# Kernel tuning notes

Hardware: AMD Instinct MI355X
Metric: run time of the kernel (lower is better)

Reference implementation:

```python
import jax, jax.numpy as jnp
import numpy as np

DIM = 768
N_HEADS = 12
HEAD_DIM = DIM // N_HEADS
HIDDEN = 4 * DIM
EPS = 1e-5


def _layernorm(x, g, b):
    m = jnp.mean(x, axis=-1, keepdims=True)
    v = jnp.mean(jnp.square(x - m), axis=-1, keepdims=True)
    return (x - m) * jax.lax.rsqrt(v + EPS) * g + b


def setup_inputs() -> dict:
    key = jax.random.key(0)
    ks = jax.random.split(key, 16)
    s = lambda fan_in: 1.0 / np.sqrt(fan_in)
    return {
        "x": jax.random.normal(ks[0], (2, 2048, DIM), dtype=jnp.float32),
        "ln1_g": jnp.ones((DIM,), jnp.float32),
        "ln1_b": jnp.zeros((DIM,), jnp.float32),
        "qkv_w": jax.random.uniform(ks[1], (DIM, 3 * DIM), jnp.float32, -s(DIM), s(DIM)),
        "qkv_b": jax.random.uniform(ks[2], (3 * DIM,), jnp.float32, -s(DIM), s(DIM)),
        "proj_w": jax.random.uniform(ks[3], (DIM, DIM), jnp.float32, -s(DIM), s(DIM)),
        "proj_b": jax.random.uniform(ks[4], (DIM,), jnp.float32, -s(DIM), s(DIM)),
        "ln2_g": jnp.ones((DIM,), jnp.float32),
        "ln2_b": jnp.zeros((DIM,), jnp.float32),
        "w1": jax.random.uniform(ks[5], (DIM, HIDDEN), jnp.float32, -s(DIM), s(DIM)),
        "b1": jax.random.uniform(ks[6], (HIDDEN,), jnp.float32, -s(DIM), s(DIM)),
        "w2": jax.random.uniform(ks[7], (HIDDEN, DIM), jnp.float32, -s(HIDDEN), s(HIDDEN)),
        "b2": jax.random.uniform(ks[8], (DIM,), jnp.float32, -s(HIDDEN), s(HIDDEN)),
    }


def reference(x, ln1_g, ln1_b, qkv_w, qkv_b, proj_w, proj_b, ln2_g, ln2_b, w1, b1, w2, b2):
    B, N, C = x.shape
    # ---- attention branch (pre-norm) ----
    h = _layernorm(x, ln1_g, ln1_b)
    qkv = (h @ qkv_w + qkv_b).reshape(B, N, 3, N_HEADS, HEAD_DIM)
    qkv = qkv.transpose(2, 0, 3, 1, 4)  # [3, B, H, N, Dh]
    q, k, v = qkv[0], qkv[1], qkv[2]
    scale = HEAD_DIM ** -0.5
    scores = jnp.einsum("bhnd,bhmd->bhnm", q, k) * scale  # [B,H,N,N]
    attn = jax.nn.softmax(scores, axis=-1)
    ctx = jnp.einsum("bhnm,bhmd->bhnd", attn, v)  # [B,H,N,Dh]
    ctx = ctx.transpose(0, 2, 1, 3).reshape(B, N, C)
    x = x + ctx @ proj_w + proj_b
    # ---- MLP branch (pre-norm) ----
    h = _layernorm(x, ln2_g, ln2_b)
    h = jax.nn.gelu(h @ w1 + b1, approximate=False)  # torch nn.GELU default = exact erf
    x = x + h @ w2 + b2
    return x
```

## Files before the change

### kernel.cpp

```cpp
#include <hip/hip_runtime.h>
#include <hip/hip_bf16.h>
#include <math.h>

#define DIM 768
#define NHEADS 12
#define HDIM 64
#define HIDDEN 3072
#define SEQ 2048
#define NTOK 4096
#define QKV3 2304

typedef __attribute__((ext_vector_type(8))) __bf16 bf16x8;
typedef __attribute__((ext_vector_type(4))) float f32x4;
typedef __attribute__((ext_vector_type(16))) float f32x16;

__device__ __forceinline__ ushort f32_bf16(float f) {
  union { float f; uint u; } c{f};
  uint u = c.u;
  u = (u + 0x7FFFu + ((u >> 16) & 1u)) >> 16;
  return (ushort)u;
}

__device__ __forceinline__ uint cvt_pk_bf16(float lo, float hi) {
  uint r;
  asm("v_cvt_pk_bf16_f32 %0, %1, %2" : "=v"(r) : "v"(lo), "v"(hi));
  return r;
}

__device__ __forceinline__ void glds16(const ushort* g, ushort* l) {
  __builtin_amdgcn_global_load_lds(
      (const __attribute__((address_space(1))) unsigned int*)(const void*)g,
      (__attribute__((address_space(3))) unsigned int*)(void*)l, 16, 0, 0);
}

union U8 { uint u[4]; bf16x8 v; };

__global__ __launch_bounds__(256) void transpose_to_bf16(
    const float* __restrict__ in, ushort* __restrict__ out, int K, int N) {
  __shared__ float tile[32][33];
  int kb = blockIdx.y * 32, nb = blockIdx.x * 32;
  int tx = threadIdx.x, ty = threadIdx.y;
#pragma unroll
  for (int i = 0; i < 32; i += 8)
    tile[ty + i][tx] = in[(size_t)(kb + ty + i) * N + nb + tx];
  __syncthreads();
#pragma unroll
  for (int i = 0; i < 32; i += 8)
    out[(size_t)(nb + ty + i) * K + kb + tx] = f32_bf16(tile[tx][ty + i]);
}

__global__ __launch_bounds__(256) void ln_bf16(
    const float* __restrict__ x, const float* __restrict__ g,
    const float* __restrict__ bta, ushort* __restrict__ out) {
  int row = blockIdx.x;
  const float* xr = x + (size_t)row * DIM;
  int t = threadIdx.x;
  float v0 = xr[t], v1 = xr[t + 256], v2 = xr[t + 512];
  float s = v0 + v1 + v2;
  float q = v0 * v0 + v1 * v1 + v2 * v2;
#pragma unroll
  for (int m = 1; m < 64; m <<= 1) {
    s += __shfl_xor(s, m);
    q += __shfl_xor(q, m);
  }
  __shared__ float ss[4], qq[4];
  int wid = t >> 6;
  if ((t & 63) == 0) { ss[wid] = s; qq[wid] = q; }
  __syncthreads();
  s = ss[0] + ss[1] + ss[2] + ss[3];
  q = qq[0] + qq[1] + qq[2] + qq[3];
  float mean = s * (1.0f / DIM);
  float var = q * (1.0f / DIM) - mean * mean;
  float rs = rsqrtf(var + 1e-5f);
  size_t o = (size_t)row * DIM;
  out[o + t]       = f32_bf16((v0 - mean) * rs * g[t]       + bta[t]);
  out[o + t + 256] = f32_bf16((v1 - mean) * rs * g[t + 256] + bta[t + 256]);
  out[o + t + 512] = f32_bf16((v2 - mean) * rs * g[t + 512] + bta[t + 512]);
}

template <int EPI>
__global__ __launch_bounds__(256, 2) void gemm_bf16(
    const ushort* __restrict__ A, const ushort* __restrict__ Bt,
    const float* __restrict__ bias, const float* __restrict__ resid,
    void* __restrict__ outv, int M, int N, int K) {
  __shared__ __align__(16) ushort As[128 * 64];
  __shared__ __align__(16) ushort Bs[128 * 64];
  int t = threadIdx.x;
  int lane = t & 63, w = t >> 6;
  int wr = w >> 1, wc = w & 1;
  int m0 = blockIdx.y * 128, n0 = blockIdx.x * 128;
  f32x4 acc[4][4] = {};
  int rl = lane & 15, g = lane >> 4, rl7 = rl & 7;

  int baseRow = w * 32 + (lane >> 3);
  int cs = (lane & 7) ^ ((lane >> 3) & 7);
  const ushort* Asrc = A + (size_t)(m0 + baseRow) * K + cs * 8;
  const ushort* Bsrc = Bt + (size_t)(n0 + baseRow) * K + cs * 8;
  ushort* Adst = &As[(w * 256 + lane) * 8];
  ushort* Bdst = &Bs[(w * 256 + lane) * 8];

  for (int k0 = 0; k0 < K; k0 += 64) {
    __syncthreads();
#pragma unroll
    for (int i = 0; i < 4; i++) {
      glds16(Asrc + (size_t)i * 8 * K + k0, Adst + i * 512);
      glds16(Bsrc + (size_t)i * 8 * K + k0, Bdst + i * 512);
    }
    __syncthreads();
    bf16x8 a[2][4], b[2][4];
#pragma unroll
    for (int kk = 0; kk < 2; kk++)
#pragma unroll
      for (int i = 0; i < 4; i++) {
        a[kk][i] = *(const bf16x8*)&As[(wr * 64 + i * 16 + rl) * 64 + ((kk * 4 + g) ^ rl7) * 8];
        b[kk][i] = *(const bf16x8*)&Bs[(wc * 64 + i * 16 + rl) * 64 + ((kk * 4 + g) ^ rl7) * 8];
      }
#pragma unroll
    for (int kk = 0; kk < 2; kk++)
#pragma unroll
      for (int i = 0; i < 4; i++)
#pragma unroll
        for (int j = 0; j < 4; j++)
          acc[i][j] = __builtin_amdgcn_mfma_f32_16x16x32_bf16(a[kk][i], b[kk][j], acc[i][j], 0, 0, 0);
  }
  int g4 = (lane >> 4) * 4;
#pragma unroll
  for (int i = 0; i < 4; i++) {
#pragma unroll
    for (int j = 0; j < 4; j++) {
      int col = n0 + wc * 64 + j * 16 + rl;
      float bval = bias[col];
#pragma unroll
      for (int r = 0; r < 4; r++) {
        int row = m0 + wr * 64 + i * 16 + g4 + r;
        float v = acc[i][j][r] + bval;
        if (EPI == 0) {
          ((ushort*)outv)[(size_t)row * N + col] = f32_bf16(v);
        } else if (EPI == 1) {
          v += resid[(size_t)row * N + col];
          ((float*)outv)[(size_t)row * N + col] = v;
        } else {
          v = 0.5f * v * (1.0f + erff(v * 0.70710678118654752f));
          ((ushort*)outv)[(size_t)row * N + col] = f32_bf16(v);
        }
      }
    }
  }
}

__global__ __launch_bounds__(256, 3) void attn_kernel(
    const ushort* __restrict__ qkv, ushort* __restrict__ ctx) {
  __shared__ __align__(16) ushort Ks[2][4096];
  __shared__ __align__(16) ushort Vt[2][4096];
  __shared__ float mml[2][2][64];
  int t = threadIdx.x, lane = t & 63, w = t >> 6;
  int qh = w & 1, kvpar = w >> 1;
  int kl = lane & 31, hi = lane >> 5;
  int qt = blockIdx.x, h = blockIdx.y, b = blockIdx.z;

  bf16x8 bq[4];
  {
    size_t qbase = (size_t)(b * SEQ + qt * 64 + qh * 32 + kl) * QKV3 + h * HDIM + hi * 8;
#pragma unroll
    for (int mi = 0; mi < 4; mi++) bq[mi] = *(const bf16x8*)(qkv + qbase + mi * 16);
  }
  f32x16 acc_o[2] = {};
  float m2 = -1e30f, lst = 0.0f;

  int pairLane = qh * 64 + lane;
  const ushort* kbase = qkv + (size_t)(b * SEQ) * QKV3 + DIM + h * HDIM;
  ushort* KsB = Ks[kvpar];
  ushort* VtB = Vt[kvpar];

  for (int it = 0; it < SEQ / 128; it++) {
    int kt = it * 2 + kvpar;
    __syncthreads();
#pragma unroll
    for (int i = 0; i < 4; i++) {
      int s = i * 128 + pairLane;
      int key = s >> 3, cc = s & 7;
      int c = cc ^ (key & 7);
      glds16(kbase + (size_t)(kt * 64 + key) * QKV3 + c * 8, &KsB[s * 8]);
    }
#pragma unroll
    for (int i = 0; i < 4; i++) {
      int s = i * 128 + pairLane;
      int key = s >> 3, c = s & 7;
      uint4 v4 = *(const uint4*)(kbase + DIM + (size_t)(kt * 64 + key) * QKV3 + c * 8);
      int co = ((key >> 3) ^ c) * 8 + (key & 7);
      uint vv[4] = {v4.x, v4.y, v4.z, v4.w};
#pragma unroll
      for (int u = 0; u < 4; u++) {
        VtB[(c * 8 + 2 * u) * 64 + co]     = (ushort)(vv[u] & 0xffffu);
        VtB[(c * 8 + 2 * u + 1) * 64 + co] = (ushort)(vv[u] >> 16);
      }
    }
    __syncthreads();

    f32x16 accs[2] = {};
#pragma unroll
    for (int ks = 0; ks < 2; ks++) {
      int key = ks * 32 + kl;
      int kswz = key & 7;
#pragma unroll
      for (int mi = 0; mi < 4; mi++) {
        bf16x8 ak = *(const bf16x8*)&KsB[key * 64 + ((2 * mi + hi) ^ kswz) * 8];
        accs[ks] = __builtin_amdgcn_mfma_f32_32x32x16_bf16(ak, bq[mi], accs[ks], 0, 0, 0);
      }
    }

    float mx = accs[0][0];
#pragma unroll
    for (int ks = 0; ks < 2; ks++)
#pragma unroll
      for (int r = 0; r < 16; r++) mx = fmaxf(mx, accs[ks][r]);
    mx = fmaxf(mx, __shfl_xor(mx, 32));
    float me = mx * 0.125f;
    if (!__all(me - m2 <= 8.0f)) {
      float newm = fmaxf(m2, me);
      float fac = __expf(m2 - newm);
      m2 = newm;
      lst *= fac;
#pragma unroll
      for (int r = 0; r < 16; r++) {
        int qrow = (r & 3) + 8 * (r >> 2) + 4 * hi;
        float fr = __shfl(fac, qrow | (lane & 32));
        acc_o[0][r] *= fr;
        acc_o[1][r] *= fr;
      }
    }
    float ps = 0.0f;
    uint PK[2][8];
#pragma unroll
    for (int ks = 0; ks < 2; ks++)
#pragma unroll
      for (int rp = 0; rp < 8; rp++) {
        float p0 = __expf(fmaf(accs[ks][2 * rp],     0.125f, -m2));
        float p1 = __expf(fmaf(accs[ks][2 * rp + 1], 0.125f, -m2));
        ps += p0 + p1;
        PK[ks][rp] = cvt_pk_bf16(p0, p1);
      }
    ps += __shfl_xor(ps, 32);
    lst += ps;

#pragma unroll
    for (int tt = 0; tt < 4; tt++) {
      const int ks = tt >> 1, tb = 4 * (tt & 1);
      uint e0 = hi ? PK[ks][tb]     : PK[ks][tb + 2];
      uint e1 = hi ? PK[ks][tb + 1] : PK[ks][tb + 3];
      uint x0 = __shfl_xor(e0, 32), x1 = __shfl_xor(e1, 32);
      uint l0 = hi ? PK[ks][tb + 2] : PK[ks][tb];
      uint l1 = hi ? PK[ks][tb + 3] : PK[ks][tb + 1];
      U8 a;
      a.u[0] = hi ? x0 : l0;
      a.u[1] = hi ? x1 : l1;
      a.u[2] = hi ? l0 : x0;
      a.u[3] = hi ? l1 : x1;
#pragma unroll
      for (int dn = 0; dn < 2; dn++) {
        int d = dn * 32 + kl;
        bf16x8 bv = *(const bf16x8*)&VtB[d * 64 + ((2 * tt + hi) ^ (d >> 3)) * 8];
        acc_o[dn] = __builtin_amdgcn_mfma_f32_32x32x16_bf16(a.v, bv, acc_o[dn], 0, 0, 0);
      }
    }
  }

  __syncthreads();
  float* obuf = (float*)(qh ? Ks[1] : Ks[0]);
  if (kvpar == 1) {
#pragma unroll
    for (int dn = 0; dn < 2; dn++)
#pragma unroll
      for (int r = 0; r < 16; r++)
        obuf[(dn * 16 + r) * 64 + lane] = acc_o[dn][r];
    mml[qh][0][lane] = m2;
    mml[qh][1][lane] = lst;
  }
  __syncthreads();
  if (kvpar == 0) {
    float mb = mml[qh][0][lane], lb = mml[qh][1][lane];
    float m = fmaxf(m2, mb);
    float fa = __expf(m2 - m), fb = __expf(mb - m);
    lst = lst * fa + lb * fb;
    float inv = 1.0f / lst;
#pragma unroll
    for (int r = 0; r < 16; r++) {
      int qrow = (r & 3) + 8 * (r >> 2) + 4 * hi;
      int src = qrow | (lane & 32);
      float far = __shfl(fa, src), fbr = __shfl(fb, src), ir = __shfl(inv, src);
      size_t row = (size_t)(b * SEQ + qt * 64 + qh * 32 + qrow);
#pragma unroll
      for (int dn = 0; dn < 2; dn++) {
        float v = (acc_o[dn][r] * far + obuf[(dn * 16 + r) * 64 + lane] * fbr) * ir;
        ctx[row * DIM + h * HDIM + dn * 32 + kl] = f32_bf16(v);
      }
    }
  }
}

extern "C" void kernel_launch(void* const* d_in, const int* in_sizes, int n_in,
                              void* d_out, int out_size, void* d_ws, size_t ws_size,
                              hipStream_t stream) {
  const float* x      = (const float*)d_in[0];
  const float* ln1_g  = (const float*)d_in[1];
  const float* ln1_b  = (const float*)d_in[2];
  const float* qkv_w  = (const float*)d_in[3];
  const float* qkv_b  = (const float*)d_in[4];
  const float* proj_w = (const float*)d_in[5];
  const float* proj_b = (const float*)d_in[6];
  const float* ln2_g  = (const float*)d_in[7];
  const float* ln2_b  = (const float*)d_in[8];
  const float* w1     = (const float*)d_in[9];
  const float* b1     = (const float*)d_in[10];
  const float* w2     = (const float*)d_in[11];
  const float* b2     = (const float*)d_in[12];
  float* out = (float*)d_out;

  char* ws = (char*)d_ws;
  size_t off = 0;
  auto alloc = [&](size_t bytes) -> void* {
    void* p = ws + off;
    off += (bytes + 255) & ~(size_t)255;
    return p;
  };
  ushort* wqkv_t  = (ushort*)alloc((size_t)QKV3 * DIM * 2);
  ushort* wproj_t = (ushort*)alloc((size_t)DIM * DIM * 2);
  ushort* w1_t    = (ushort*)alloc((size_t)HIDDEN * DIM * 2);
  ushort* w2_t    = (ushort*)alloc((size_t)DIM * HIDDEN * 2);
  ushort* hbuf    = (ushort*)alloc((size_t)NTOK * DIM * 2);
  ushort* ubuf    = (ushort*)alloc((size_t)NTOK * HIDDEN * 2);
  ushort* ctx     = (ushort*)alloc((size_t)NTOK * DIM * 2);
  float*  x1      = (float*)alloc((size_t)NTOK * DIM * 4);
  ushort* qkvbuf = ubuf;
  ushort* m1     = ubuf;

  transpose_to_bf16<<<dim3(QKV3 / 32, DIM / 32), dim3(32, 8), 0, stream>>>(qkv_w, wqkv_t, DIM, QKV3);
  transpose_to_bf16<<<dim3(DIM / 32, DIM / 32), dim3(32, 8), 0, stream>>>(proj_w, wproj_t, DIM, DIM);
  transpose_to_bf16<<<dim3(HIDDEN / 32, DIM / 32), dim3(32, 8), 0, stream>>>(w1, w1_t, DIM, HIDDEN);
  transpose_to_bf16<<<dim3(DIM / 32, HIDDEN / 32), dim3(32, 8), 0, stream>>>(w2, w2_t, HIDDEN, DIM);

  ln_bf16<<<NTOK, 256, 0, stream>>>(x, ln1_g, ln1_b, hbuf);
  gemm_bf16<0><<<dim3(QKV3 / 128, NTOK / 128), 256, 0, stream>>>(
      hbuf, wqkv_t, qkv_b, nullptr, qkvbuf, NTOK, QKV3, DIM);
  attn_kernel<<<dim3(SEQ / 64, NHEADS, 2), 256, 0, stream>>>(qkvbuf, ctx);
  gemm_bf16<1><<<dim3(DIM / 128, NTOK / 128), 256, 0, stream>>>(
      ctx, wproj_t, proj_b, x, x1, NTOK, DIM, DIM);
  ln_bf16<<<NTOK, 256, 0, stream>>>(x1, ln2_g, ln2_b, hbuf);
  gemm_bf16<2><<<dim3(HIDDEN / 128, NTOK / 128), 256, 0, stream>>>(
      hbuf, w1_t, b1, nullptr, m1, NTOK, HIDDEN, DIM);
  gemm_bf16<1><<<dim3(DIM / 128, NTOK / 128), 256, 0, stream>>>(
      m1, w2_t, b2, x1, out, NTOK, DIM, HIDDEN);
}
```

Baseline: 214.8 us.

## Split-K the MLP down-projection into three partial GEMMs with a reduce kernel

The final w2 GEMM (K=3072) originally launched only 192 blocks. It now runs as three K-slices on a z-grid, writing bf16 partials into freed workspace buffers. A new elementwise kernel sums the partials with the bias and residual. Separately, the GEMM launch bound is raised to 3 waves per SIMD and s_setprio is wrapped around the attention MFMA sections to favour matrix work. The split costs an extra launch, extra partial traffic, and some precision from rounding the partials to bf16.

```diff
diff --git a/kernel.cpp b/kernel.cpp
--- a/kernel.cpp
+++ b/kernel.cpp
@@ -19,6 +19,11 @@
   uint u = c.u;
   u = (u + 0x7FFFu + ((u >> 16) & 1u)) >> 16;
   return (ushort)u;
+}
+
+__device__ __forceinline__ float bf16_f32(ushort u) {
+  union { uint u; float f; } c{(uint)u << 16};
+  return c.f;
 }
 
 __device__ __forceinline__ uint cvt_pk_bf16(float lo, float hi) {
@@ -79,23 +84,25 @@
 }
 
 template <int EPI>
-__global__ __launch_bounds__(256, 2) void gemm_bf16(
+__global__ __launch_bounds__(256, 3) void gemm_bf16(
     const ushort* __restrict__ A, const ushort* __restrict__ Bt,
     const float* __restrict__ bias, const float* __restrict__ resid,
-    void* __restrict__ outv, int M, int N, int K) {
+    void* __restrict__ outv, int M, int N, int K, int lda, int ldb,
+    ushort* __restrict__ p0, ushort* __restrict__ p1, ushort* __restrict__ p2) {
   __shared__ __align__(16) ushort As[128 * 64];
   __shared__ __align__(16) ushort Bs[128 * 64];
   int t = threadIdx.x;
   int lane = t & 63, w = t >> 6;
   int wr = w >> 1, wc = w & 1;
   int m0 = blockIdx.y * 128, n0 = blockIdx.x * 128;
+  int kb = blockIdx.z * K;
   f32x4 acc[4][4] = {};
   int rl = lane & 15, g = lane >> 4, rl7 = rl & 7;
 
   int baseRow = w * 32 + (lane >> 3);
   int cs = (lane & 7) ^ ((lane >> 3) & 7);
-  const ushort* Asrc = A + (size_t)(m0 + baseRow) * K + cs * 8;
-  const ushort* Bsrc = Bt + (size_t)(n0 + baseRow) * K + cs * 8;
+  const ushort* Asrc = A + (size_t)(m0 + baseRow) * lda + kb + cs * 8;
+  const ushort* Bsrc = Bt + (size_t)(n0 + baseRow) * ldb + kb + cs * 8;
   ushort* Adst = &As[(w * 256 + lane) * 8];
   ushort* Bdst = &Bs[(w * 256 + lane) * 8];
 
@@ -103,8 +110,8 @@
     __syncthreads();
 #pragma unroll
     for (int i = 0; i < 4; i++) {
-      glds16(Asrc + (size_t)i * 8 * K + k0, Adst + i * 512);
-      glds16(Bsrc + (size_t)i * 8 * K + k0, Bdst + i * 512);
+      glds16(Asrc + (size_t)i * 8 * lda + k0, Adst + i * 512);
+      glds16(Bsrc + (size_t)i * 8 * ldb + k0, Bdst + i * 512);
     }
     __syncthreads();
     bf16x8 a[2][4], b[2][4];
@@ -123,13 +130,14 @@
         for (int j = 0; j < 4; j++)
           acc[i][j] = __builtin_amdgcn_mfma_f32_16x16x32_bf16(a[kk][i], b[kk][j], acc[i][j], 0, 0, 0);
   }
+  ushort* pz = (blockIdx.z == 0) ? p0 : ((blockIdx.z == 1) ? p1 : p2);
   int g4 = (lane >> 4) * 4;
 #pragma unroll
   for (int i = 0; i < 4; i++) {
 #pragma unroll
     for (int j = 0; j < 4; j++) {
       int col = n0 + wc * 64 + j * 16 + rl;
-      float bval = bias[col];
+      float bval = (EPI == 3) ? 0.0f : bias[col];
 #pragma unroll
       for (int r = 0; r < 4; r++) {
         int row = m0 + wr * 64 + i * 16 + g4 + r;
@@ -139,13 +147,34 @@
         } else if (EPI == 1) {
           v += resid[(size_t)row * N + col];
           ((float*)outv)[(size_t)row * N + col] = v;
-        } else {
+        } else if (EPI == 2) {
           v = 0.5f * v * (1.0f + erff(v * 0.70710678118654752f));
           ((ushort*)outv)[(size_t)row * N + col] = f32_bf16(v);
+        } else {
+          pz[(size_t)row * N + col] = f32_bf16(v);
         }
       }
     }
   }
+}
+
+__global__ __launch_bounds__(256) void reduce3_kernel(
+    const ushort* __restrict__ p0, const ushort* __restrict__ p1,
+    const ushort* __restrict__ p2, const float* __restrict__ x1,
+    const float* __restrict__ bias, float* __restrict__ out) {
+  int i = blockIdx.x * 256 + threadIdx.x;
+  int col = (i * 4) % DIM;
+  const ushort4 a0 = ((const ushort4*)p0)[i];
+  const ushort4 a1 = ((const ushort4*)p1)[i];
+  const ushort4 a2 = ((const ushort4*)p2)[i];
+  const float4 xv = ((const float4*)x1)[i];
+  const float4 bv = *(const float4*)&bias[col];
+  float4 o;
+  o.x = xv.x + bv.x + bf16_f32(a0.x) + bf16_f32(a1.x) + bf16_f32(a2.x);
+  o.y = xv.y + bv.y + bf16_f32(a0.y) + bf16_f32(a1.y) + bf16_f32(a2.y);
+  o.z = xv.z + bv.z + bf16_f32(a0.z) + bf16_f32(a1.z) + bf16_f32(a2.z);
+  o.w = xv.w + bv.w + bf16_f32(a0.w) + bf16_f32(a1.w) + bf16_f32(a2.w);
+  ((float4*)out)[i] = o;
 }
 
 __global__ __launch_bounds__(256, 3) void attn_kernel(
@@ -198,6 +227,7 @@
     __syncthreads();
 
     f32x16 accs[2] = {};
+    __builtin_amdgcn_s_setprio(1);
 #pragma unroll
     for (int ks = 0; ks < 2; ks++) {
       int key = ks * 32 + kl;
@@ -208,6 +238,7 @@
         accs[ks] = __builtin_amdgcn_mfma_f32_32x32x16_bf16(ak, bq[mi], accs[ks], 0, 0, 0);
       }
     }
+    __builtin_amdgcn_s_setprio(0);
 
     float mx = accs[0][0];
 #pragma unroll
@@ -256,12 +287,14 @@
       a.u[1] = hi ? x1 : l1;
       a.u[2] = hi ? l0 : x0;
       a.u[3] = hi ? l1 : x1;
+      __builtin_amdgcn_s_setprio(1);
 #pragma unroll
       for (int dn = 0; dn < 2; dn++) {
         int d = dn * 32 + kl;
         bf16x8 bv = *(const bf16x8*)&VtB[d * 64 + ((2 * tt + hi) ^ (d >> 3)) * 8];
         acc_o[dn] = __builtin_amdgcn_mfma_f32_32x32x16_bf16(a.v, bv, acc_o[dn], 0, 0, 0);
       }
+      __builtin_amdgcn_s_setprio(0);
     }
   }
 
@@ -333,6 +366,9 @@
   float*  x1      = (float*)alloc((size_t)NTOK * DIM * 4);
   ushort* qkvbuf = ubuf;
   ushort* m1     = ubuf;
+  ushort* part0 = (ushort*)ws;
+  ushort* part1 = hbuf;
+  ushort* part2 = ctx;
 
   transpose_to_bf16<<<dim3(QKV3 / 32, DIM / 32), dim3(32, 8), 0, stream>>>(qkv_w, wqkv_t, DIM, QKV3);
   transpose_to_bf16<<<dim3(DIM / 32, DIM / 32), dim3(32, 8), 0, stream>>>(proj_w, wproj_t, DIM, DIM);
@@ -341,13 +377,19 @@
 
   ln_bf16<<<NTOK, 256, 0, stream>>>(x, ln1_g, ln1_b, hbuf);
   gemm_bf16<0><<<dim3(QKV3 / 128, NTOK / 128), 256, 0, stream>>>(
-      hbuf, wqkv_t, qkv_b, nullptr, qkvbuf, NTOK, QKV3, DIM);
+      hbuf, wqkv_t, qkv_b, nullptr, qkvbuf, NTOK, QKV3, DIM, DIM, DIM,
+      nullptr, nullptr, nullptr);
   attn_kernel<<<dim3(SEQ / 64, NHEADS, 2), 256, 0, stream>>>(qkvbuf, ctx);
   gemm_bf16<1><<<dim3(DIM / 128, NTOK / 128), 256, 0, stream>>>(
-      ctx, wproj_t, proj_b, x, x1, NTOK, DIM, DIM);
+      ctx, wproj_t, proj_b, x, x1, NTOK, DIM, DIM, DIM, DIM,
+      nullptr, nullptr, nullptr);
   ln_bf16<<<NTOK, 256, 0, stream>>>(x1, ln2_g, ln2_b, hbuf);
   gemm_bf16<2><<<dim3(HIDDEN / 128, NTOK / 128), 256, 0, stream>>>(
-      hbuf, w1_t, b1, nullptr, m1, NTOK, HIDDEN, DIM);
-  gemm_bf16<1><<<dim3(DIM / 128, NTOK / 128), 256, 0, stream>>>(
-      m1, w2_t, b2, x1, out, NTOK, DIM, HIDDEN);
-}
+      hbuf, w1_t, b1, nullptr, m1, NTOK, HIDDEN, DIM, DIM, DIM,
+      nullptr, nullptr, nullptr);
+  gemm_bf16<3><<<dim3(DIM / 128, NTOK / 128, 3), 256, 0, stream>>>(
+      m1, w2_t, nullptr, nullptr, nullptr, NTOK, DIM, HIDDEN / 3, HIDDEN, HIDDEN,
+      part0, part1, part2);
+  reduce3_kernel<<<NTOK * DIM / 4 / 256, 256, 0, stream>>>(
+      part0, part1, part2, x1, b2, out);
+}
```

Measured after the change: 199.1 us. 1.08x faster.
